# Kernel tuning notes

Measured on AMD Instinct MI355X. Metric: run time of the kernel, lower is better.

Reference implementation:

```python
import jax, jax.numpy as jnp
import numpy as np

C = 3          # num_classes
A = 3          # anchors per cell
IMG = 256.0    # image size used to build grid anchors
EPS = 1e-6


def make_anchors(H, W, n_a=A):
    """Grid anchors in (H, W, A) order, matching the pred permute order."""
    stride = IMG / H
    ys, xs = np.meshgrid(np.arange(H), np.arange(W), indexing='ij')
    cx = (xs + 0.5) * stride
    cy = (ys + 0.5) * stride
    sizes = np.array([2.0, 3.0, 4.0]) * stride
    out = np.zeros((H, W, n_a, 4), np.float32)
    for a in range(n_a):
        h = sizes[a] * 0.5
        out[..., a, 0] = cx - h
        out[..., a, 1] = cy - h
        out[..., a, 2] = cx + h
        out[..., a, 3] = cy + h
    return jnp.asarray(out.reshape(-1, 4))


def setup_inputs() -> dict:
    key = jax.random.key(0)
    ks = jax.random.split(key, 6)
    B, M = 32, 20
    inp = {}
    for i, H in enumerate([128, 64, 32]):
        inp[f'pred{i+1}'] = jax.random.normal(ks[i], (B, A * (5 + C), H, H), jnp.float32)
        inp[f'anchors{i+1}'] = make_anchors(H, H)
    ctr = jax.random.uniform(ks[3], (B, M, 2), minval=32.0, maxval=IMG - 32.0)
    wh = jax.random.uniform(ks[4], (B, M, 2), minval=16.0, maxval=80.0)
    inp['gt_boxes'] = jnp.concatenate([ctr - 0.5 * wh, ctr + 0.5 * wh], axis=-1)
    inp['gt_labels'] = jax.random.randint(ks[5], (B, M), 0, C)
    return inp


def _iou(anchors, gt):  # [N,4], [M,4] -> [N,M]
    lt = jnp.maximum(anchors[:, None, :2], gt[None, :, :2])
    rb = jnp.minimum(anchors[:, None, 2:], gt[None, :, 2:])
    wh = jnp.clip(rb - lt, 0.0)
    inter = wh[..., 0] * wh[..., 1]
    aa = (anchors[:, 2] - anchors[:, 0]) * (anchors[:, 3] - anchors[:, 1])
    ag = (gt[:, 2] - gt[:, 0]) * (gt[:, 3] - gt[:, 1])
    return inter / (aa[:, None] + ag[None, :] - inter + EPS)


def _to_cxcywh(box):
    x1, y1, x2, y2 = box[..., 0], box[..., 1], box[..., 2], box[..., 3]
    w = jnp.maximum(x2 - x1, EPS)
    h = jnp.maximum(y2 - y1, EPS)
    return x1 + 0.5 * w, y1 + 0.5 * h, w, h


def _encode(gt, anc):  # (tx, ty, tw, th) as in DetectionLoss.encode_boxes
    gcx, gcy, gw, gh = _to_cxcywh(gt)
    acx, acy, aw, ah = _to_cxcywh(anc)
    tx = (gcx - acx) / (aw + EPS)
    ty = (gcy - acy) / (ah + EPS)
    tw = jnp.log((gw + EPS) / (aw + EPS))
    th = jnp.log((gh + EPS) / (ah + EPS))
    return jnp.stack([tx, ty, tw, th], axis=-1)


def _mine(loss, pos, neg, ratio=3):
    """Hard-negative mining: top-(3*max(num_pos,1)) negatives by obj loss."""
    N = loss.shape[0]
    k = ratio * jnp.maximum(pos.sum(), 1)
    neg_loss = jnp.where(neg, loss, -jnp.inf)
    order = jnp.argsort(-neg_loss)
    rank = jnp.zeros(N, jnp.int32).at[order].set(jnp.arange(N, dtype=jnp.int32))
    return (rank < k) & neg


def _per_image(pred, anchors, boxes, labels):
    # pred: [N, 5+C]; anchors: [N, 4]; boxes: [M, 4]; labels: [M]
    ious = _iou(anchors, boxes)
    best_iou = ious.max(axis=1)
    best_gt = ious.argmax(axis=1)
    pos = best_iou >= 0.5
    neg = best_iou < 0.3
    matched_boxes = boxes[best_gt]
    matched_labels = jnp.where(pos, labels[best_gt] + 1, 0)

    pred_loc, pred_obj, pred_cls = pred[:, :4], pred[:, 4], pred[:, 5:]

    # BCE-with-logits, per anchor
    obj_t = pos.astype(pred.dtype)
    obj_loss = jnp.maximum(pred_obj, 0.0) - pred_obj * obj_t + jnp.log1p(jnp.exp(-jnp.abs(pred_obj)))
    sel_neg = _mine(jax.lax.stop_gradient(obj_loss), pos, neg)
    obj_mask = pos | sel_neg
    obj_sum = jnp.sum(jnp.where(obj_mask, obj_loss, 0.0))

    # Cross-entropy on positives (labels shifted back by -1)
    logp = jax.nn.log_softmax(pred_cls, axis=-1)
    tgt = jnp.clip(matched_labels - 1, 0, C - 1)
    ce = -jnp.take_along_axis(logp, tgt[:, None], axis=1)[:, 0]
    cls_sum = jnp.sum(jnp.where(pos, ce, 0.0))

    # Smooth-L1 on encoded deltas for positives
    d = pred_loc - _encode(matched_boxes, anchors)
    sl1 = jnp.where(jnp.abs(d) < 1.0, 0.5 * d * d, jnp.abs(d) - 0.5).sum(axis=-1)
    loc_sum = jnp.sum(jnp.where(pos, sl1, 0.0))

    return obj_sum, obj_mask.sum(), cls_sum, loc_sum, pos.sum()


def reference(pred1, pred2, pred3, anchors1, anchors2, anchors3, gt_boxes, gt_labels):
    tot = [jnp.float32(0.0), jnp.int32(0), jnp.float32(0.0), jnp.float32(0.0), jnp.int32(0)]
    for pred, anc in [(pred1, anchors1), (pred2, anchors2), (pred3, anchors3)]:
        B, ch, H, W = pred.shape
        # [B, A*(5+C), H, W] -> [B, H*W*A, 5+C]  (same permute as torch)
        p = pred.reshape(B, A, 5 + C, H, W).transpose(0, 3, 4, 1, 2).reshape(B, -1, 5 + C)
        res = jax.vmap(_per_image, in_axes=(0, None, 0, 0))(p, anc, gt_boxes, gt_labels)
        tot = [t + r.sum() for t, r in zip(tot, res)]
    obj_sum, obj_den, cls_sum, loc_sum, n_pos = tot
    pos_norm = jnp.maximum(n_pos, 1).astype(jnp.float32)
    obj_norm = jnp.maximum(obj_den, 1).astype(jnp.float32)
    loss_obj = obj_sum / obj_norm
    loss_cls = cls_sum / pos_norm
    loss_loc = loc_sum / pos_norm
    loss_total = 1.0 * loss_obj + 1.0 * loss_cls + 2.0 * loss_loc
    return jnp.stack([loss_obj, loss_cls, loss_loc, loss_total])
```

## Files before the change

### kernel.cpp

```cpp
#include <hip/hip_runtime.h>
#include <hip/hip_bf16.h>
#include <math.h>

#define M_GT 20
#define EPSF 1e-6f
#define N_TOT 64512
#define B_IMG 32
#define NPAIR 96
#define MBINS 4096
#define TIE_CAP 2048
#define MT 1024
#define SENT_BITS 0xFF800000u

__device__ __forceinline__ unsigned keyof(unsigned bits) {
    return (bits & 0x80000000u) ? ~bits : (bits | 0x80000000u);
}
__device__ __forceinline__ float softplus_ref(float x) {
    return fmaxf(x, 0.f) + log1pf(expf(-fabsf(x)));
}

template<int H, int SEG_OFF>
__device__ __forceinline__ void match_scale(
    const float* __restrict__ pred,
    const float* __restrict__ gt_boxes,
    const int*   __restrict__ gt_labels,
    float* __restrict__ neg_key,
    int*   __restrict__ pos_cnt,
    float* __restrict__ sums,
    int pixblk, int b, int pair)
{
    constexpr int HW = H * H;
    constexpr float STRIDE = 256.0f / (float)H;
    constexpr int NROWS = 256 / H;
    const int tid = threadIdx.x;
    const int pix = pixblk * 256 + tid;

    __shared__ float4 s_box[M_GT];
    __shared__ float  s_ag[M_GT];
    __shared__ int    s_lab[M_GT];
    __shared__ int    s_nk;

    if (tid < 64) {
        bool keep = false;
        float4 g = make_float4(0.f, 0.f, 0.f, 0.f);
        int lab = 0;
        if (tid < M_GT) {
            g   = reinterpret_cast<const float4*>(gt_boxes)[b * M_GT + tid];
            lab = gt_labels[b * M_GT + tid];
            const int y0 = (pixblk * 256) / H;
            const float lo = ((float)y0 + 0.5f) * STRIDE - 2.0f * STRIDE;
            const float hi = ((float)(y0 + NROWS - 1) + 0.5f) * STRIDE + 2.0f * STRIDE;
            keep = (g.y < hi) && (g.w > lo);
        }
        unsigned long long m = __ballot(keep);
        if (keep) {
            int posi = __popcll(m & ((1ull << tid) - 1ull));
            s_box[posi] = g;
            s_ag[posi]  = (g.z - g.x) * (g.w - g.y);
            s_lab[posi] = lab;
        }
        if (tid == 0) s_nk = __popcll(m);
    }
    __syncthreads();
    const int nk = s_nk;

    const int x = pix % H;
    const int y = pix / H;
    const float cx = ((float)x + 0.5f) * STRIDE;
    const float cy = ((float)y + 0.5f) * STRIDE;
    const size_t pbase = (size_t)b * 24 * HW + pix;

    const float axL1 = cx - 2.0f * STRIDE, ayL1 = cy - 2.0f * STRIDE;
    const float axL2 = cx + 2.0f * STRIDE, ayL2 = cy + 2.0f * STRIDE;

    float best[3] = {-1.f, -1.f, -1.f};
    int   bj[3]   = {0, 0, 0};

    for (int j = 0; j < nk; ++j) {
        const float4 gb = s_box[j];
        const float glx = fmaxf(axL1, gb.x), gly = fmaxf(ayL1, gb.y);
        const float grx = fminf(axL2, gb.z), gry = fminf(ayL2, gb.w);
        if (grx <= glx || gry <= gly) continue;
        const float ag = s_ag[j];
        #pragma unroll
        for (int a = 0; a < 3; ++a) {
            const float half = 0.5f * ((float)(a + 2) * STRIDE);
            const float ax1 = cx - half, ay1 = cy - half;
            const float ax2 = cx + half, ay2 = cy + half;
            const float aa = (ax2 - ax1) * (ay2 - ay1);
            float lx = fmaxf(ax1, gb.x);
            float ly = fmaxf(ay1, gb.y);
            float rx = fminf(ax2, gb.z);
            float ry = fminf(ay2, gb.w);
            float w  = fmaxf(rx - lx, 0.f);
            float h  = fmaxf(ry - ly, 0.f);
            float inter = w * h;
            float iou = inter / (aa + ag - inter + EPSF);
            if (iou > best[a]) { best[a] = iou; bj[a] = j; }
        }
    }

    float l_obj = 0.f, l_cls = 0.f, l_loc = 0.f;
    int l_pos = 0;

    #pragma unroll
    for (int a = 0; a < 3; ++a) {
        const float ba = fmaxf(best[a], 0.0f);
        const bool pos = (ba >= 0.5f);
        const bool neg = (ba < 0.3f);

        const float po = pred[pbase + (size_t)(a * 8 + 4) * HW];
        neg_key[(size_t)b * N_TOT + SEG_OFF + a * HW + pix] =
            neg ? po : __uint_as_float(SENT_BITS);

        if (pos) {
            const int j = bj[a];
            const float half = 0.5f * ((float)(a + 2) * STRIDE);
            const float ax1 = cx - half, ay1 = cy - half;
            const float ax2 = cx + half, ay2 = cy + half;
            l_pos += 1;
            l_obj += fmaxf(po, 0.f) - po + log1pf(expf(-fabsf(po)));
            float c0 = pred[pbase + (size_t)(a * 8 + 5) * HW];
            float c1 = pred[pbase + (size_t)(a * 8 + 6) * HW];
            float c2 = pred[pbase + (size_t)(a * 8 + 7) * HW];
            float m2 = fmaxf(c0, fmaxf(c1, c2));
            float lse = m2 + logf(expf(c0 - m2) + expf(c1 - m2) + expf(c2 - m2));
            int tgt = s_lab[j];
            float lt = (tgt == 0) ? c0 : ((tgt == 1) ? c1 : c2);
            l_cls += lse - lt;
            float4 gb = s_box[j];
            float gw = fmaxf(gb.z - gb.x, EPSF), gh = fmaxf(gb.w - gb.y, EPSF);
            float gcx = gb.x + 0.5f * gw, gcy = gb.y + 0.5f * gh;
            float aw = fmaxf(ax2 - ax1, EPSF), ah = fmaxf(ay2 - ay1, EPSF);
            float acx = ax1 + 0.5f * aw, acy = ay1 + 0.5f * ah;
            float tx = (gcx - acx) / (aw + EPSF);
            float ty = (gcy - acy) / (ah + EPSF);
            float tw = logf((gw + EPSF) / (aw + EPSF));
            float th = logf((gh + EPSF) / (ah + EPSF));
            float p0 = pred[pbase + (size_t)(a * 8 + 0) * HW];
            float p1 = pred[pbase + (size_t)(a * 8 + 1) * HW];
            float p2 = pred[pbase + (size_t)(a * 8 + 2) * HW];
            float p3 = pred[pbase + (size_t)(a * 8 + 3) * HW];
            float d0 = p0 - tx, d1 = p1 - ty, d2 = p2 - tw, d3 = p3 - th;
            float ad;
            ad = fabsf(d0); l_loc += (ad < 1.f) ? 0.5f * d0 * d0 : ad - 0.5f;
            ad = fabsf(d1); l_loc += (ad < 1.f) ? 0.5f * d1 * d1 : ad - 0.5f;
            ad = fabsf(d2); l_loc += (ad < 1.f) ? 0.5f * d2 * d2 : ad - 0.5f;
            ad = fabsf(d3); l_loc += (ad < 1.f) ? 0.5f * d3 * d3 : ad - 0.5f;
        }
    }

    if (l_pos) {
        atomicAdd(&pos_cnt[pair], l_pos);
        atomicAdd(&sums[0], l_obj);
        atomicAdd(&sums[1], l_cls);
        atomicAdd(&sums[2], l_loc);
    }
}

__global__ __launch_bounds__(256) void match_kernel(
    const float* __restrict__ pred1, const float* __restrict__ pred2,
    const float* __restrict__ pred3, const float* __restrict__ gt_boxes,
    const int* __restrict__ gt_labels, float* __restrict__ neg_key,
    int* __restrict__ pos_cnt, float* __restrict__ sums)
{
    const int b  = blockIdx.y;
    const int bx = blockIdx.x;
    if (bx < 64)
        match_scale<128, 0>(pred1, gt_boxes, gt_labels, neg_key, pos_cnt, sums, bx, b, b * 3 + 0);
    else if (bx < 80)
        match_scale<64, 49152>(pred2, gt_boxes, gt_labels, neg_key, pos_cnt, sums, bx - 64, b, b * 3 + 1);
    else
        match_scale<32, 61440>(pred3, gt_boxes, gt_labels, neg_key, pos_cnt, sums, bx - 80, b, b * 3 + 2);
}

__device__ __forceinline__ int suffix_scan_1024(int x, int* wtot, int tid, int* tot_out) {
    const int lane = tid & 63, w = tid >> 6;
    int v = x;
    #pragma unroll
    for (int off = 1; off < 64; off <<= 1) {
        int u = __shfl_down(v, off);
        if (lane + off < 64) v += u;
    }
    __syncthreads();
    if (lane == 0) wtot[w] = v;
    __syncthreads();
    int add = 0, tot = 0;
    #pragma unroll
    for (int j = 0; j < 16; ++j) {
        int t = wtot[j];
        tot += t;
        if (j > w) add += t;
    }
    *tot_out = tot;
    return v + add;
}

__global__ __launch_bounds__(MT) void mine_kernel(
    const float* __restrict__ neg_key,
    int*   pos_cnt,
    float* sums,
    int*   done,
    float* sel_sum,
    int*   sel_cnt,
    float* __restrict__ out)
{
    const int p = blockIdx.x;
    const int s = p % 3;
    const int b = p / 3;
    const int seg_off = (s == 0) ? 0 : (s == 1) ? 49152 : 61440;
    const int len4    = ((s == 0) ? 49152 : (s == 1) ? 12288 : 3072) >> 2;
    const float4* seg4 =
        reinterpret_cast<const float4*>(neg_key + (size_t)b * N_TOT + seg_off);
    const int tid = threadIdx.x;

    __shared__ int   hist[MBINS];
    __shared__ int   wtot[16];
    __shared__ float ties[TIE_CAP];
    __shared__ float wpart[16];
    __shared__ int s_tcnt, s_tbin, s_kr, s_binA, s_krA, s_binB, s_krB, s_last;

    for (int i = tid; i < MBINS; i += MT) hist[i] = 0;
    if (tid == 0) s_tcnt = 0;
    __syncthreads();

    auto proc1 = [&](float x) {
        unsigned ub = __float_as_uint(x);
        if (ub != SENT_BITS) atomicAdd(&hist[keyof(ub) >> 20], 1);
    };
    {
        int i = tid;
        for (; i + 3 * MT < len4; i += 4 * MT) {
            float4 a0 = seg4[i], a1 = seg4[i + MT], a2 = seg4[i + 2 * MT], a3 = seg4[i + 3 * MT];
            proc1(a0.x); proc1(a0.y); proc1(a0.z); proc1(a0.w);
            proc1(a1.x); proc1(a1.y); proc1(a1.z); proc1(a1.w);
            proc1(a2.x); proc1(a2.y); proc1(a2.z); proc1(a2.w);
            proc1(a3.x); proc1(a3.y); proc1(a3.z); proc1(a3.w);
        }
        for (; i < len4; i += MT) {
            float4 a0 = seg4[i];
            proc1(a0.x); proc1(a0.y); proc1(a0.z); proc1(a0.w);
        }
    }
    __syncthreads();

    const int b0 = tid * 4;
    const int my = hist[b0] + hist[b0 + 1] + hist[b0 + 2] + hist[b0 + 3];
    int nneg;
    const int incl = suffix_scan_1024(my, wtot, tid, &nneg);
    const int k = 3 * max(pos_cnt[p], 1);
    const bool ta = (k >= nneg);
    if (!ta && (incl - my) < k && k <= incl) {
        int cg = incl - my;
        for (int bin = b0 + 3; bin >= b0; --bin) {
            int c = hist[bin];
            if (cg < k && k <= cg + c) { s_tbin = bin; s_kr = k - cg; break; }
            cg += c;
        }
    }
    __syncthreads();
    const int tbin = ta ? 0 : s_tbin;

    float acc = 0.f;
    auto proc3 = [&](float x) {
        unsigned ub = __float_as_uint(x);
        if (ub == SENT_BITS) return;
        int bin = (int)(keyof(ub) >> 20);
        if (ta || bin > tbin) acc += softplus_ref(x);
        else if (bin == tbin) {
            int idx = atomicAdd(&s_tcnt, 1);
            if (idx < TIE_CAP) ties[idx] = x;
        }
    };
    {
        int i = tid;
        for (; i + 3 * MT < len4; i += 4 * MT) {
            float4 a0 = seg4[i], a1 = seg4[i + MT], a2 = seg4[i + 2 * MT], a3 = seg4[i + 3 * MT];
            proc3(a0.x); proc3(a0.y); proc3(a0.z); proc3(a0.w);
            proc3(a1.x); proc3(a1.y); proc3(a1.z); proc3(a1.w);
            proc3(a2.x); proc3(a2.y); proc3(a2.z); proc3(a2.w);
            proc3(a3.x); proc3(a3.y); proc3(a3.z); proc3(a3.w);
        }
        for (; i < len4; i += MT) {
            float4 a0 = seg4[i];
            proc3(a0.x); proc3(a0.y); proc3(a0.z); proc3(a0.w);
        }
    }
    #pragma unroll
    for (int off = 32; off > 0; off >>= 1) acc += __shfl_down(acc, off);
    __syncthreads();
    if ((tid & 63) == 0) wpart[tid >> 6] = acc;
    __syncthreads();
    float blocksum = 0.f;
    if (tid == 0) {
        #pragma unroll
        for (int j = 0; j < 16; ++j) blocksum += wpart[j];
    }

    float extra = 0.f;
    const int selcnt = ta ? nneg : k;
    if (!ta) {
        const int m  = min(s_tcnt, TIE_CAP);
        const int kr = s_kr;
        hist[tid] = 0;
        __syncthreads();
        for (int i = tid; i < m; i += MT)
            atomicAdd(&hist[(keyof(__float_as_uint(ties[i])) >> 10) & 1023], 1);
        __syncthreads();
        {
            int myA = hist[tid], totA;
            int inclA = suffix_scan_1024(myA, wtot, tid, &totA);
            if ((inclA - myA) < kr && kr <= inclA) { s_binA = tid; s_krA = kr - (inclA - myA); }
        }
        __syncthreads();
        const int binA = s_binA, krA = s_krA;
        hist[tid] = 0;
        __syncthreads();
        for (int i = tid; i < m; i += MT) {
            unsigned key = keyof(__float_as_uint(ties[i]));
            if (((key >> 10) & 1023) == (unsigned)binA) atomicAdd(&hist[key & 1023], 1);
        }
        __syncthreads();
        {
            int myB = hist[tid], totB;
            int inclB = suffix_scan_1024(myB, wtot, tid, &totB);
            if ((inclB - myB) < krA && krA <= inclB) { s_binB = tid; s_krB = krA - (inclB - myB); }
        }
        __syncthreads();
        const unsigned tkey = (((unsigned)tbin) << 20) | (((unsigned)binA) << 10)
                            | (unsigned)s_binB;
        float acc2 = 0.f;
        for (int i = tid; i < m; i += MT) {
            float x = ties[i];
            if (keyof(__float_as_uint(x)) > tkey) acc2 += softplus_ref(x);
        }
        #pragma unroll
        for (int off = 32; off > 0; off >>= 1) acc2 += __shfl_down(acc2, off);
        __syncthreads();
        if ((tid & 63) == 0) wpart[tid >> 6] = acc2;
        __syncthreads();
        if (tid == 0) {
            float e2 = 0.f;
            #pragma unroll
            for (int j = 0; j < 16; ++j) e2 += wpart[j];
            const unsigned tb2 = (tkey & 0x80000000u) ? (tkey & 0x7FFFFFFFu) : ~tkey;
            extra = e2 + (float)s_krB * softplus_ref(__uint_as_float(tb2));
        }
    }

    if (tid == 0) {
        atomicExch(&sel_sum[p], blocksum + extra);
        atomicExch(&sel_cnt[p], selcnt);
        __threadfence();
        int old = atomicAdd(done, 1);
        s_last = (old == NPAIR - 1) ? 1 : 0;
    }
    __syncthreads();
    if (s_last) {
        __threadfence();
        float fs = 0.f; int c1 = 0, c2 = 0;
        if (tid < NPAIR) {
            fs = atomicAdd(&sel_sum[tid], 0.0f);
            c1 = atomicAdd(&pos_cnt[tid], 0);
            c2 = atomicAdd(&sel_cnt[tid], 0);
        }
        #pragma unroll
        for (int off = 32; off > 0; off >>= 1) {
            fs += __shfl_down(fs, off);
            c1 += __shfl_down(c1, off);
            c2 += __shfl_down(c2, off);
        }
        __shared__ float f2[16]; __shared__ int a2[16], b2[16];
        if ((tid & 63) == 0) { f2[tid >> 6] = fs; a2[tid >> 6] = c1; b2[tid >> 6] = c2; }
        __syncthreads();
        if (tid == 0) {
            float obj    = atomicAdd(&sums[0], 0.0f) + f2[0] + f2[1];
            float clsum  = atomicAdd(&sums[1], 0.0f);
            float locsum = atomicAdd(&sums[2], 0.0f);
            int np  = a2[0] + a2[1];
            int den = np + b2[0] + b2[1];
            float pn = (float)max(np, 1);
            float on = (float)max(den, 1);
            float lo = obj / on, lc = clsum / pn, ll = locsum / pn;
            out[0] = lo; out[1] = lc; out[2] = ll;
            out[3] = lo + lc + 2.0f * ll;
        }
    }
}

extern "C" void kernel_launch(void* const* d_in, const int* in_sizes, int n_in,
                              void* d_out, int out_size, void* d_ws, size_t ws_size,
                              hipStream_t stream) {
    const float* pred1     = (const float*)d_in[0];
    const float* pred2     = (const float*)d_in[2];
    const float* pred3     = (const float*)d_in[4];
    const float* gt_boxes  = (const float*)d_in[6];
    const int*   gt_labels = (const int*)d_in[7];

    char* ws = (char*)d_ws;
    float* sums    = (float*)(ws + 0);
    int*   pos_cnt = (int*)  (ws + 16);
    int*   done    = (int*)  (ws + 400);
    float* sel_sum = (float*)(ws + 512);
    int*   sel_cnt = (int*)  (ws + 896);
    float* neg_key = (float*)(ws + 1280);

    hipMemsetAsync(d_ws, 0, 512, stream);

    match_kernel<<<dim3(84, B_IMG), 256, 0, stream>>>(
        pred1, pred2, pred3, gt_boxes, gt_labels, neg_key, pos_cnt, sums);

    mine_kernel<<<NPAIR, MT, 0, stream>>>(
        neg_key, pos_cnt, sums, done, sel_sum, sel_cnt, (float*)d_out);
}
```

Measured before the change: 137.5 us.

## Fuse anchor matching and hard-negative mining into one per-pair kernel

Replaces the separate match and mine kernels with a single kernel where each block handles one (image, scale) pair. The block does the anchor matching itself, builds the negative histogram in shared memory, and re-reads the objectness logits directly from pred instead of going through a global neg_key buffer. Per-pair partial sums go to slots, and a tiny final kernel reduces them, which removes the memset, the global atomics and the last-block-done protocol. In exchange the matching runs on only 96 blocks with serial chunks per block, so the large-scale pairs carry much more work and fewer CUs are busy.

```diff
diff --git a/kernel.cpp b/kernel.cpp
--- a/kernel.cpp
+++ b/kernel.cpp
@@ -4,174 +4,15 @@
 
 #define M_GT 20
 #define EPSF 1e-6f
-#define N_TOT 64512
 #define B_IMG 32
 #define NPAIR 96
-#define MBINS 4096
 #define TIE_CAP 2048
-#define MT 1024
-#define SENT_BITS 0xFF800000u
 
 __device__ __forceinline__ unsigned keyof(unsigned bits) {
     return (bits & 0x80000000u) ? ~bits : (bits | 0x80000000u);
 }
 __device__ __forceinline__ float softplus_ref(float x) {
     return fmaxf(x, 0.f) + log1pf(expf(-fabsf(x)));
-}
-
-template<int H, int SEG_OFF>
-__device__ __forceinline__ void match_scale(
-    const float* __restrict__ pred,
-    const float* __restrict__ gt_boxes,
-    const int*   __restrict__ gt_labels,
-    float* __restrict__ neg_key,
-    int*   __restrict__ pos_cnt,
-    float* __restrict__ sums,
-    int pixblk, int b, int pair)
-{
-    constexpr int HW = H * H;
-    constexpr float STRIDE = 256.0f / (float)H;
-    constexpr int NROWS = 256 / H;
-    const int tid = threadIdx.x;
-    const int pix = pixblk * 256 + tid;
-
-    __shared__ float4 s_box[M_GT];
-    __shared__ float  s_ag[M_GT];
-    __shared__ int    s_lab[M_GT];
-    __shared__ int    s_nk;
-
-    if (tid < 64) {
-        bool keep = false;
-        float4 g = make_float4(0.f, 0.f, 0.f, 0.f);
-        int lab = 0;
-        if (tid < M_GT) {
-            g   = reinterpret_cast<const float4*>(gt_boxes)[b * M_GT + tid];
-            lab = gt_labels[b * M_GT + tid];
-            const int y0 = (pixblk * 256) / H;
-            const float lo = ((float)y0 + 0.5f) * STRIDE - 2.0f * STRIDE;
-            const float hi = ((float)(y0 + NROWS - 1) + 0.5f) * STRIDE + 2.0f * STRIDE;
-            keep = (g.y < hi) && (g.w > lo);
-        }
-        unsigned long long m = __ballot(keep);
-        if (keep) {
-            int posi = __popcll(m & ((1ull << tid) - 1ull));
-            s_box[posi] = g;
-            s_ag[posi]  = (g.z - g.x) * (g.w - g.y);
-            s_lab[posi] = lab;
-        }
-        if (tid == 0) s_nk = __popcll(m);
-    }
-    __syncthreads();
-    const int nk = s_nk;
-
-    const int x = pix % H;
-    const int y = pix / H;
-    const float cx = ((float)x + 0.5f) * STRIDE;
-    const float cy = ((float)y + 0.5f) * STRIDE;
-    const size_t pbase = (size_t)b * 24 * HW + pix;
-
-    const float axL1 = cx - 2.0f * STRIDE, ayL1 = cy - 2.0f * STRIDE;
-    const float axL2 = cx + 2.0f * STRIDE, ayL2 = cy + 2.0f * STRIDE;
-
-    float best[3] = {-1.f, -1.f, -1.f};
-    int   bj[3]   = {0, 0, 0};
-
-    for (int j = 0; j < nk; ++j) {
-        const float4 gb = s_box[j];
-        const float glx = fmaxf(axL1, gb.x), gly = fmaxf(ayL1, gb.y);
-        const float grx = fminf(axL2, gb.z), gry = fminf(ayL2, gb.w);
-        if (grx <= glx || gry <= gly) continue;
-        const float ag = s_ag[j];
-        #pragma unroll
-        for (int a = 0; a < 3; ++a) {
-            const float half = 0.5f * ((float)(a + 2) * STRIDE);
-            const float ax1 = cx - half, ay1 = cy - half;
-            const float ax2 = cx + half, ay2 = cy + half;
-            const float aa = (ax2 - ax1) * (ay2 - ay1);
-            float lx = fmaxf(ax1, gb.x);
-            float ly = fmaxf(ay1, gb.y);
-            float rx = fminf(ax2, gb.z);
-            float ry = fminf(ay2, gb.w);
-            float w  = fmaxf(rx - lx, 0.f);
-            float h  = fmaxf(ry - ly, 0.f);
-            float inter = w * h;
-            float iou = inter / (aa + ag - inter + EPSF);
-            if (iou > best[a]) { best[a] = iou; bj[a] = j; }
-        }
-    }
-
-    float l_obj = 0.f, l_cls = 0.f, l_loc = 0.f;
-    int l_pos = 0;
-
-    #pragma unroll
-    for (int a = 0; a < 3; ++a) {
-        const float ba = fmaxf(best[a], 0.0f);
-        const bool pos = (ba >= 0.5f);
-        const bool neg = (ba < 0.3f);
-
-        const float po = pred[pbase + (size_t)(a * 8 + 4) * HW];
-        neg_key[(size_t)b * N_TOT + SEG_OFF + a * HW + pix] =
-            neg ? po : __uint_as_float(SENT_BITS);
-
-        if (pos) {
-            const int j = bj[a];
-            const float half = 0.5f * ((float)(a + 2) * STRIDE);
-            const float ax1 = cx - half, ay1 = cy - half;
-            const float ax2 = cx + half, ay2 = cy + half;
-            l_pos += 1;
-            l_obj += fmaxf(po, 0.f) - po + log1pf(expf(-fabsf(po)));
-            float c0 = pred[pbase + (size_t)(a * 8 + 5) * HW];
-            float c1 = pred[pbase + (size_t)(a * 8 + 6) * HW];
-            float c2 = pred[pbase + (size_t)(a * 8 + 7) * HW];
-            float m2 = fmaxf(c0, fmaxf(c1, c2));
-            float lse = m2 + logf(expf(c0 - m2) + expf(c1 - m2) + expf(c2 - m2));
-            int tgt = s_lab[j];
-            float lt = (tgt == 0) ? c0 : ((tgt == 1) ? c1 : c2);
-            l_cls += lse - lt;
-            float4 gb = s_box[j];
-            float gw = fmaxf(gb.z - gb.x, EPSF), gh = fmaxf(gb.w - gb.y, EPSF);
-            float gcx = gb.x + 0.5f * gw, gcy = gb.y + 0.5f * gh;
-            float aw = fmaxf(ax2 - ax1, EPSF), ah = fmaxf(ay2 - ay1, EPSF);
-            float acx = ax1 + 0.5f * aw, acy = ay1 + 0.5f * ah;
-            float tx = (gcx - acx) / (aw + EPSF);
-            float ty = (gcy - acy) / (ah + EPSF);
-            float tw = logf((gw + EPSF) / (aw + EPSF));
-            float th = logf((gh + EPSF) / (ah + EPSF));
-            float p0 = pred[pbase + (size_t)(a * 8 + 0) * HW];
-            float p1 = pred[pbase + (size_t)(a * 8 + 1) * HW];
-            float p2 = pred[pbase + (size_t)(a * 8 + 2) * HW];
-            float p3 = pred[pbase + (size_t)(a * 8 + 3) * HW];
-            float d0 = p0 - tx, d1 = p1 - ty, d2 = p2 - tw, d3 = p3 - th;
-            float ad;
-            ad = fabsf(d0); l_loc += (ad < 1.f) ? 0.5f * d0 * d0 : ad - 0.5f;
-            ad = fabsf(d1); l_loc += (ad < 1.f) ? 0.5f * d1 * d1 : ad - 0.5f;
-            ad = fabsf(d2); l_loc += (ad < 1.f) ? 0.5f * d2 * d2 : ad - 0.5f;
-            ad = fabsf(d3); l_loc += (ad < 1.f) ? 0.5f * d3 * d3 : ad - 0.5f;
-        }
-    }
-
-    if (l_pos) {
-        atomicAdd(&pos_cnt[pair], l_pos);
-        atomicAdd(&sums[0], l_obj);
-        atomicAdd(&sums[1], l_cls);
-        atomicAdd(&sums[2], l_loc);
-    }
-}
-
-__global__ __launch_bounds__(256) void match_kernel(
-    const float* __restrict__ pred1, const float* __restrict__ pred2,
-    const float* __restrict__ pred3, const float* __restrict__ gt_boxes,
-    const int* __restrict__ gt_labels, float* __restrict__ neg_key,
-    int* __restrict__ pos_cnt, float* __restrict__ sums)
-{
-    const int b  = blockIdx.y;
-    const int bx = blockIdx.x;
-    if (bx < 64)
-        match_scale<128, 0>(pred1, gt_boxes, gt_labels, neg_key, pos_cnt, sums, bx, b, b * 3 + 0);
-    else if (bx < 80)
-        match_scale<64, 49152>(pred2, gt_boxes, gt_labels, neg_key, pos_cnt, sums, bx - 64, b, b * 3 + 1);
-    else
-        match_scale<32, 61440>(pred3, gt_boxes, gt_labels, neg_key, pos_cnt, sums, bx - 80, b, b * 3 + 2);
 }
 
 __device__ __forceinline__ int suffix_scan_1024(int x, int* wtot, int tid, int* tot_out) {
@@ -196,127 +37,197 @@
     return v + add;
 }
 
-__global__ __launch_bounds__(MT) void mine_kernel(
-    const float* __restrict__ neg_key,
-    int*   pos_cnt,
-    float* sums,
-    int*   done,
-    float* sel_sum,
-    int*   sel_cnt,
-    float* __restrict__ out)
+__device__ __forceinline__ float wave_reduce_f(float v) {
+    #pragma unroll
+    for (int off = 32; off > 0; off >>= 1) v += __shfl_down(v, off);
+    return v;
+}
+
+template<int H, int NCH>
+__device__ __forceinline__ void pair_impl(
+    const float* __restrict__ pred,
+    const float4* __restrict__ gtb,
+    const int*   __restrict__ gtl,
+    float* __restrict__ slot,
+    int* hist, float* ties, float4* sbox, float* sag, int* slab, int* snk,
+    int* wtot, float* wpart, int* smisc)
 {
-    const int p = blockIdx.x;
-    const int s = p % 3;
-    const int b = p / 3;
-    const int seg_off = (s == 0) ? 0 : (s == 1) ? 49152 : 61440;
-    const int len4    = ((s == 0) ? 49152 : (s == 1) ? 12288 : 3072) >> 2;
-    const float4* seg4 =
-        reinterpret_cast<const float4*>(neg_key + (size_t)b * N_TOT + seg_off);
+    constexpr int HW = H * H;
+    constexpr float STRIDE = 256.0f / (float)H;
+    constexpr int RPC = 1024 / H;
     const int tid = threadIdx.x;
-
-    __shared__ int   hist[MBINS];
-    __shared__ int   wtot[16];
-    __shared__ float ties[TIE_CAP];
-    __shared__ float wpart[16];
-    __shared__ int s_tcnt, s_tbin, s_kr, s_binA, s_krA, s_binB, s_krB, s_last;
-
-    for (int i = tid; i < MBINS; i += MT) hist[i] = 0;
-    if (tid == 0) s_tcnt = 0;
-    __syncthreads();
-
-    auto proc1 = [&](float x) {
-        unsigned ub = __float_as_uint(x);
-        if (ub != SENT_BITS) atomicAdd(&hist[keyof(ub) >> 20], 1);
-    };
-    {
-        int i = tid;
-        for (; i + 3 * MT < len4; i += 4 * MT) {
-            float4 a0 = seg4[i], a1 = seg4[i + MT], a2 = seg4[i + 2 * MT], a3 = seg4[i + 3 * MT];
-            proc1(a0.x); proc1(a0.y); proc1(a0.z); proc1(a0.w);
-            proc1(a1.x); proc1(a1.y); proc1(a1.z); proc1(a1.w);
-            proc1(a2.x); proc1(a2.y); proc1(a2.z); proc1(a2.w);
-            proc1(a3.x); proc1(a3.y); proc1(a3.z); proc1(a3.w);
-        }
-        for (; i < len4; i += MT) {
-            float4 a0 = seg4[i];
-            proc1(a0.x); proc1(a0.y); proc1(a0.z); proc1(a0.w);
-        }
-    }
-    __syncthreads();
+    const int lane = tid & 63, wv = tid >> 6;
+
+    for (int i = tid; i < 4096; i += 1024) hist[i] = 0;
+    if (tid == 0) smisc[0] = 0;
+
+    if (wv < NCH) {
+        bool keep = false;
+        float4 g = make_float4(0.f, 0.f, 0.f, 0.f);
+        int lab = 0;
+        if (lane < M_GT) {
+            g = gtb[lane]; lab = gtl[lane];
+            const float lo = ((float)(wv * RPC) + 0.5f) * STRIDE - 2.0f * STRIDE;
+            const float hi = ((float)(wv * RPC + RPC - 1) + 0.5f) * STRIDE + 2.0f * STRIDE;
+            keep = (g.y < hi) && (g.w > lo);
+        }
+        unsigned long long m = __ballot(keep);
+        if (keep) {
+            int posi = __popcll(m & ((1ull << lane) - 1ull));
+            sbox[wv * M_GT + posi] = g;
+            sag [wv * M_GT + posi] = (g.z - g.x) * (g.w - g.y);
+            slab[wv * M_GT + posi] = lab;
+        }
+        if (lane == 0) snk[wv] = __popcll(m);
+    }
+    __syncthreads();
+
+    unsigned long long negbits = 0ull;
+    float l_obj = 0.f, l_cls = 0.f, l_loc = 0.f;
+    int l_pos = 0;
+
+    for (int c = 0; c < NCH; ++c) {
+        const int pix = c * 1024 + tid;
+        const int x = pix & (H - 1);
+        const int y = pix / H;
+        const float cx = ((float)x + 0.5f) * STRIDE;
+        const float cy = ((float)y + 0.5f) * STRIDE;
+        const int nk = snk[c];
+        const float axL1 = cx - 2.f * STRIDE, ayL1 = cy - 2.f * STRIDE;
+        const float axL2 = cx + 2.f * STRIDE, ayL2 = cy + 2.f * STRIDE;
+
+        float best[3] = {-1.f, -1.f, -1.f};
+        int bj[3] = {0, 0, 0};
+        for (int j = 0; j < nk; ++j) {
+            const float4 gb = sbox[c * M_GT + j];
+            const float glx = fmaxf(axL1, gb.x), gly = fmaxf(ayL1, gb.y);
+            const float grx = fminf(axL2, gb.z), gry = fminf(ayL2, gb.w);
+            if (grx <= glx || gry <= gly) continue;
+            const float ag = sag[c * M_GT + j];
+            #pragma unroll
+            for (int a = 0; a < 3; ++a) {
+                const float half = 0.5f * ((float)(a + 2) * STRIDE);
+                const float ax1 = cx - half, ay1 = cy - half;
+                const float ax2 = cx + half, ay2 = cy + half;
+                const float aa = (ax2 - ax1) * (ay2 - ay1);
+                float lx = fmaxf(ax1, gb.x);
+                float ly = fmaxf(ay1, gb.y);
+                float rx = fminf(ax2, gb.z);
+                float ry = fminf(ay2, gb.w);
+                float w  = fmaxf(rx - lx, 0.f);
+                float h  = fmaxf(ry - ly, 0.f);
+                float inter = w * h;
+                float iou = inter / (aa + ag - inter + EPSF);
+                if (iou > best[a]) { best[a] = iou; bj[a] = j; }
+            }
+        }
+
+        #pragma unroll
+        for (int a = 0; a < 3; ++a) {
+            const float ba = fmaxf(best[a], 0.f);
+            const bool pos = (ba >= 0.5f);
+            const bool neg = (ba < 0.3f);
+            const float po = pred[(size_t)(a * 8 + 4) * HW + pix];
+            if (neg) {
+                negbits |= (1ull << (c * 3 + a));
+                atomicAdd(&hist[keyof(__float_as_uint(po)) >> 20], 1);
+            }
+            if (pos) {
+                const int j = bj[a];
+                const float half = 0.5f * ((float)(a + 2) * STRIDE);
+                const float ax1 = cx - half, ay1 = cy - half;
+                const float ax2 = cx + half, ay2 = cy + half;
+                l_pos += 1;
+                l_obj += fmaxf(po, 0.f) - po + log1pf(expf(-fabsf(po)));
+                float c0 = pred[(size_t)(a * 8 + 5) * HW + pix];
+                float c1 = pred[(size_t)(a * 8 + 6) * HW + pix];
+                float c2 = pred[(size_t)(a * 8 + 7) * HW + pix];
+                float m2 = fmaxf(c0, fmaxf(c1, c2));
+                float lse = m2 + logf(expf(c0 - m2) + expf(c1 - m2) + expf(c2 - m2));
+                int tgt = slab[c * M_GT + j];
+                float lt = (tgt == 0) ? c0 : ((tgt == 1) ? c1 : c2);
+                l_cls += lse - lt;
+                float4 gb = sbox[c * M_GT + j];
+                float gw = fmaxf(gb.z - gb.x, EPSF), gh = fmaxf(gb.w - gb.y, EPSF);
+                float gcx = gb.x + 0.5f * gw, gcy = gb.y + 0.5f * gh;
+                float aw = fmaxf(ax2 - ax1, EPSF), ah = fmaxf(ay2 - ay1, EPSF);
+                float acx = ax1 + 0.5f * aw, acy = ay1 + 0.5f * ah;
+                float tx = (gcx - acx) / (aw + EPSF);
+                float ty = (gcy - acy) / (ah + EPSF);
+                float tw = logf((gw + EPSF) / (aw + EPSF));
+                float th = logf((gh + EPSF) / (ah + EPSF));
+                float p0 = pred[(size_t)(a * 8 + 0) * HW + pix];
+                float p1 = pred[(size_t)(a * 8 + 1) * HW + pix];
+                float p2 = pred[(size_t)(a * 8 + 2) * HW + pix];
+                float p3 = pred[(size_t)(a * 8 + 3) * HW + pix];
+                float d0 = p0 - tx, d1 = p1 - ty, d2 = p2 - tw, d3 = p3 - th;
+                float ad;
+                ad = fabsf(d0); l_loc += (ad < 1.f) ? 0.5f * d0 * d0 : ad - 0.5f;
+                ad = fabsf(d1); l_loc += (ad < 1.f) ? 0.5f * d1 * d1 : ad - 0.5f;
+                ad = fabsf(d2); l_loc += (ad < 1.f) ? 0.5f * d2 * d2 : ad - 0.5f;
+                ad = fabsf(d3); l_loc += (ad < 1.f) ? 0.5f * d3 * d3 : ad - 0.5f;
+            }
+        }
+    }
+    __syncthreads();
+
+    int postot;
+    suffix_scan_1024(l_pos, wtot, tid, &postot);
+    const int k = 3 * max(postot, 1);
 
     const int b0 = tid * 4;
     const int my = hist[b0] + hist[b0 + 1] + hist[b0 + 2] + hist[b0 + 3];
     int nneg;
     const int incl = suffix_scan_1024(my, wtot, tid, &nneg);
-    const int k = 3 * max(pos_cnt[p], 1);
     const bool ta = (k >= nneg);
     if (!ta && (incl - my) < k && k <= incl) {
         int cg = incl - my;
         for (int bin = b0 + 3; bin >= b0; --bin) {
-            int c = hist[bin];
-            if (cg < k && k <= cg + c) { s_tbin = bin; s_kr = k - cg; break; }
-            cg += c;
-        }
-    }
-    __syncthreads();
-    const int tbin = ta ? 0 : s_tbin;
+            int cc = hist[bin];
+            if (cg < k && k <= cg + cc) { smisc[1] = bin; smisc[2] = k - cg; break; }
+            cg += cc;
+        }
+    }
+    __syncthreads();
+    const int tbin = ta ? 0 : smisc[1];
 
     float acc = 0.f;
-    auto proc3 = [&](float x) {
-        unsigned ub = __float_as_uint(x);
-        if (ub == SENT_BITS) return;
-        int bin = (int)(keyof(ub) >> 20);
-        if (ta || bin > tbin) acc += softplus_ref(x);
-        else if (bin == tbin) {
-            int idx = atomicAdd(&s_tcnt, 1);
-            if (idx < TIE_CAP) ties[idx] = x;
-        }
-    };
-    {
-        int i = tid;
-        for (; i + 3 * MT < len4; i += 4 * MT) {
-            float4 a0 = seg4[i], a1 = seg4[i + MT], a2 = seg4[i + 2 * MT], a3 = seg4[i + 3 * MT];
-            proc3(a0.x); proc3(a0.y); proc3(a0.z); proc3(a0.w);
-            proc3(a1.x); proc3(a1.y); proc3(a1.z); proc3(a1.w);
-            proc3(a2.x); proc3(a2.y); proc3(a2.z); proc3(a2.w);
-            proc3(a3.x); proc3(a3.y); proc3(a3.z); proc3(a3.w);
-        }
-        for (; i < len4; i += MT) {
-            float4 a0 = seg4[i];
-            proc3(a0.x); proc3(a0.y); proc3(a0.z); proc3(a0.w);
-        }
-    }
-    #pragma unroll
-    for (int off = 32; off > 0; off >>= 1) acc += __shfl_down(acc, off);
-    __syncthreads();
-    if ((tid & 63) == 0) wpart[tid >> 6] = acc;
-    __syncthreads();
-    float blocksum = 0.f;
-    if (tid == 0) {
+    for (int c = 0; c < NCH; ++c) {
         #pragma unroll
-        for (int j = 0; j < 16; ++j) blocksum += wpart[j];
-    }
+        for (int a = 0; a < 3; ++a) {
+            if (negbits & (1ull << (c * 3 + a))) {
+                const float v = pred[(size_t)(a * 8 + 4) * HW + c * 1024 + tid];
+                const int bin = (int)(keyof(__float_as_uint(v)) >> 20);
+                if (ta || bin > tbin) acc += softplus_ref(v);
+                else if (bin == tbin) {
+                    int idx = atomicAdd(&smisc[0], 1);
+                    if (idx < TIE_CAP) ties[idx] = v;
+                }
+            }
+        }
+    }
+    __syncthreads();
 
     float extra = 0.f;
     const int selcnt = ta ? nneg : k;
     if (!ta) {
-        const int m  = min(s_tcnt, TIE_CAP);
-        const int kr = s_kr;
+        const int m  = min(smisc[0], TIE_CAP);
+        const int kr = smisc[2];
         hist[tid] = 0;
         __syncthreads();
-        for (int i = tid; i < m; i += MT)
+        for (int i = tid; i < m; i += 1024)
             atomicAdd(&hist[(keyof(__float_as_uint(ties[i])) >> 10) & 1023], 1);
         __syncthreads();
         {
             int myA = hist[tid], totA;
             int inclA = suffix_scan_1024(myA, wtot, tid, &totA);
-            if ((inclA - myA) < kr && kr <= inclA) { s_binA = tid; s_krA = kr - (inclA - myA); }
-        }
-        __syncthreads();
-        const int binA = s_binA, krA = s_krA;
+            if ((inclA - myA) < kr && kr <= inclA) { smisc[3] = tid; smisc[4] = kr - (inclA - myA); }
+        }
+        __syncthreads();
+        const int binA = smisc[3], krA = smisc[4];
         hist[tid] = 0;
         __syncthreads();
-        for (int i = tid; i < m; i += MT) {
+        for (int i = tid; i < m; i += 1024) {
             unsigned key = keyof(__float_as_uint(ties[i]));
             if (((key >> 10) & 1023) == (unsigned)binA) atomicAdd(&hist[key & 1023], 1);
         }
@@ -324,67 +235,115 @@
         {
             int myB = hist[tid], totB;
             int inclB = suffix_scan_1024(myB, wtot, tid, &totB);
-            if ((inclB - myB) < krA && krA <= inclB) { s_binB = tid; s_krB = krA - (inclB - myB); }
+            if ((inclB - myB) < krA && krA <= inclB) { smisc[5] = tid; smisc[6] = krA - (inclB - myB); }
         }
         __syncthreads();
         const unsigned tkey = (((unsigned)tbin) << 20) | (((unsigned)binA) << 10)
-                            | (unsigned)s_binB;
+                            | (unsigned)smisc[5];
         float acc2 = 0.f;
-        for (int i = tid; i < m; i += MT) {
-            float x = ties[i];
-            if (keyof(__float_as_uint(x)) > tkey) acc2 += softplus_ref(x);
-        }
-        #pragma unroll
-        for (int off = 32; off > 0; off >>= 1) acc2 += __shfl_down(acc2, off);
-        __syncthreads();
-        if ((tid & 63) == 0) wpart[tid >> 6] = acc2;
+        for (int i = tid; i < m; i += 1024) {
+            float xv = ties[i];
+            if (keyof(__float_as_uint(xv)) > tkey) acc2 += softplus_ref(xv);
+        }
+        acc2 = wave_reduce_f(acc2);
+        __syncthreads();
+        if (lane == 0) wpart[wv] = acc2;
         __syncthreads();
         if (tid == 0) {
             float e2 = 0.f;
             #pragma unroll
-            for (int j = 0; j < 16; ++j) e2 += wpart[j];
+            for (int j2 = 0; j2 < 16; ++j2) e2 += wpart[j2];
             const unsigned tb2 = (tkey & 0x80000000u) ? (tkey & 0x7FFFFFFFu) : ~tkey;
-            extra = e2 + (float)s_krB * softplus_ref(__uint_as_float(tb2));
-        }
-    }
-
+            extra = e2 + (float)smisc[6] * softplus_ref(__uint_as_float(tb2));
+        }
+    }
+
+    float r0 = wave_reduce_f(acc);
+    float r1 = wave_reduce_f(l_obj);
+    float r2 = wave_reduce_f(l_cls);
+    float r3 = wave_reduce_f(l_loc);
+    __syncthreads();
+    if (lane == 0) { wpart[wv] = r0; wpart[16 + wv] = r1; wpart[32 + wv] = r2; wpart[48 + wv] = r3; }
+    __syncthreads();
     if (tid == 0) {
-        atomicExch(&sel_sum[p], blocksum + extra);
-        atomicExch(&sel_cnt[p], selcnt);
-        __threadfence();
-        int old = atomicAdd(done, 1);
-        s_last = (old == NPAIR - 1) ? 1 : 0;
-    }
-    __syncthreads();
-    if (s_last) {
-        __threadfence();
-        float fs = 0.f; int c1 = 0, c2 = 0;
-        if (tid < NPAIR) {
-            fs = atomicAdd(&sel_sum[tid], 0.0f);
-            c1 = atomicAdd(&pos_cnt[tid], 0);
-            c2 = atomicAdd(&sel_cnt[tid], 0);
-        }
+        float S0 = 0.f, S1 = 0.f, S2 = 0.f, S3 = 0.f;
         #pragma unroll
-        for (int off = 32; off > 0; off >>= 1) {
-            fs += __shfl_down(fs, off);
-            c1 += __shfl_down(c1, off);
-            c2 += __shfl_down(c2, off);
-        }
-        __shared__ float f2[16]; __shared__ int a2[16], b2[16];
-        if ((tid & 63) == 0) { f2[tid >> 6] = fs; a2[tid >> 6] = c1; b2[tid >> 6] = c2; }
-        __syncthreads();
-        if (tid == 0) {
-            float obj    = atomicAdd(&sums[0], 0.0f) + f2[0] + f2[1];
-            float clsum  = atomicAdd(&sums[1], 0.0f);
-            float locsum = atomicAdd(&sums[2], 0.0f);
-            int np  = a2[0] + a2[1];
-            int den = np + b2[0] + b2[1];
-            float pn = (float)max(np, 1);
-            float on = (float)max(den, 1);
-            float lo = obj / on, lc = clsum / pn, ll = locsum / pn;
-            out[0] = lo; out[1] = lc; out[2] = ll;
-            out[3] = lo + lc + 2.0f * ll;
-        }
+        for (int j2 = 0; j2 < 16; ++j2) {
+            S0 += wpart[j2]; S1 += wpart[16 + j2]; S2 += wpart[32 + j2]; S3 += wpart[48 + j2];
+        }
+        slot[0] = S0 + extra;
+        slot[1] = (float)selcnt;
+        slot[2] = (float)postot;
+        slot[3] = S1;
+        slot[4] = S2;
+        slot[5] = S3;
+    }
+}
+
+__global__ __launch_bounds__(1024) void fused_kernel(
+    const float* __restrict__ p1, const float* __restrict__ p2,
+    const float* __restrict__ p3, const float* __restrict__ gt_boxes,
+    const int* __restrict__ gt_labels, float* __restrict__ slots)
+{
+    __shared__ int    hist[4096];
+    __shared__ float  ties[TIE_CAP];
+    __shared__ float4 sbox[16 * M_GT];
+    __shared__ float  sag [16 * M_GT];
+    __shared__ int    slab[16 * M_GT];
+    __shared__ int    snk [16];
+    __shared__ int    wtot[16];
+    __shared__ float  wpart[64];
+    __shared__ int    smisc[8];
+
+    const int p = blockIdx.x;
+    const int b = p / 3, s = p % 3;
+    const float4* gtb = reinterpret_cast<const float4*>(gt_boxes) + b * M_GT;
+    const int* gtl = gt_labels + b * M_GT;
+    float* slot = slots + p * 8;
+
+    if (s == 0)
+        pair_impl<128, 16>(p1 + (size_t)b * 24 * 128 * 128, gtb, gtl, slot,
+                           hist, ties, sbox, sag, slab, snk, wtot, wpart, smisc);
+    else if (s == 1)
+        pair_impl<64, 4>(p2 + (size_t)b * 24 * 64 * 64, gtb, gtl, slot,
+                         hist, ties, sbox, sag, slab, snk, wtot, wpart, smisc);
+    else
+        pair_impl<32, 1>(p3 + (size_t)b * 24 * 32 * 32, gtb, gtl, slot,
+                         hist, ties, sbox, sag, slab, snk, wtot, wpart, smisc);
+}
+
+__global__ __launch_bounds__(128) void final_kernel(
+    const float* __restrict__ slots, float* __restrict__ out)
+{
+    const int tid = threadIdx.x;
+    float ss = 0.f, sc = 0.f, pp = 0.f, oo = 0.f, cc = 0.f, ll = 0.f;
+    if (tid < NPAIR) {
+        const float* s = slots + tid * 8;
+        ss = s[0]; sc = s[1]; pp = s[2]; oo = s[3]; cc = s[4]; ll = s[5];
+    }
+    #pragma unroll
+    for (int off = 32; off > 0; off >>= 1) {
+        ss += __shfl_down(ss, off); sc += __shfl_down(sc, off);
+        pp += __shfl_down(pp, off); oo += __shfl_down(oo, off);
+        cc += __shfl_down(cc, off); ll += __shfl_down(ll, off);
+    }
+    __shared__ float sh[12];
+    if ((tid & 63) == 0) {
+        int w = tid >> 6;
+        sh[w * 6 + 0] = ss; sh[w * 6 + 1] = sc; sh[w * 6 + 2] = pp;
+        sh[w * 6 + 3] = oo; sh[w * 6 + 4] = cc; sh[w * 6 + 5] = ll;
+    }
+    __syncthreads();
+    if (tid == 0) {
+        float SS = sh[0] + sh[6],  SC = sh[1] + sh[7],  P = sh[2] + sh[8];
+        float O  = sh[3] + sh[9],  C  = sh[4] + sh[10], L = sh[5] + sh[11];
+        float pn = fmaxf(P, 1.f);
+        float on = fmaxf(P + SC, 1.f);
+        float lo = (O + SS) / on;
+        float lc = C / pn;
+        float l2 = L / pn;
+        out[0] = lo; out[1] = lc; out[2] = l2;
+        out[3] = lo + lc + 2.0f * l2;
     }
 }
 
@@ -397,19 +356,10 @@
     const float* gt_boxes  = (const float*)d_in[6];
     const int*   gt_labels = (const int*)d_in[7];
 
-    char* ws = (char*)d_ws;
-    float* sums    = (float*)(ws + 0);
-    int*   pos_cnt = (int*)  (ws + 16);
-    int*   done    = (int*)  (ws + 400);
-    float* sel_sum = (float*)(ws + 512);
-    int*   sel_cnt = (int*)  (ws + 896);
-    float* neg_key = (float*)(ws + 1280);
-
-    hipMemsetAsync(d_ws, 0, 512, stream);
-
-    match_kernel<<<dim3(84, B_IMG), 256, 0, stream>>>(
-        pred1, pred2, pred3, gt_boxes, gt_labels, neg_key, pos_cnt, sums);
-
-    mine_kernel<<<NPAIR, MT, 0, stream>>>(
-        neg_key, pos_cnt, sums, done, sel_sum, sel_cnt, (float*)d_out);
-}
+    float* slots = (float*)d_ws;
+
+    fused_kernel<<<NPAIR, 1024, 0, stream>>>(
+        pred1, pred2, pred3, gt_boxes, gt_labels, slots);
+
+    final_kernel<<<1, 128, 0, stream>>>(slots, (float*)d_out);
+}
```

After: 166.7 us. +21.2%, slower.
